# Optimization experiments

Measured on AMD Instinct MI355X. Metric: run time of the kernel, lower is better.

The kernel has to match this reference:

```python
import jax, jax.numpy as jnp
import numpy as np

T = 16384      # total packed tokens
C = 1024       # d_model
H = 16         # n_head
HD = C // H    # head dim = 64
N_SEG = 32     # number of equal varlen segments
SEG = T // N_SEG


def setup_inputs() -> dict:
    key = jax.random.key(0)
    k1, k2, k3 = jax.random.split(key, 3)
    x = jax.random.normal(k1, (T, C), dtype=jnp.float32)
    w_attn = jax.random.normal(k2, (C, 3 * C), dtype=jnp.float32) * (1.0 / np.sqrt(C))
    w_proj = jax.random.normal(k3, (C, C), dtype=jnp.float32) * (1.0 / np.sqrt(C))
    # boundary indices for torch.tensor_split -> 32 equal segments of SEG tokens
    split_sections = (jnp.arange(1, N_SEG) * SEG).astype(jnp.int64)
    return {"x": x, "w_attn": w_attn, "w_proj": w_proj, "split_sections": split_sections}


def reference(x, w_attn, w_proj, split_sections):
    # x: [T, C] packed tokens; split_sections: 31 boundaries -> 32 equal segments
    n_seg = int(np.asarray(split_sections).shape[0]) + 1
    seg = x.shape[0] // n_seg
    qkv = x @ w_attn                                   # [T, 3C]
    q, k, v = jnp.split(qkv, 3, axis=-1)               # each [T, C]

    def heads(t):
        # [T, C] -> [H, n_seg, seg, HD]  (block-diagonal segment layout)
        return t.reshape(x.shape[0], H, HD).transpose(1, 0, 2).reshape(H, n_seg, seg, HD)

    q, k, v = heads(q), heads(k), heads(v)
    scale = 1.0 / np.sqrt(HD)
    att = jnp.einsum('hnqd,hnkd->hnqk', q, k) * scale  # [H, n_seg, seg, seg]
    att = jax.nn.softmax(att, axis=-1)
    y = jnp.einsum('hnqk,hnkd->hnqd', att, v)          # [H, n_seg, seg, HD]
    y = y.reshape(H, x.shape[0], HD).transpose(1, 0, 2).reshape(x.shape[0], C)
    return y @ w_proj                                  # [T, C]
```

## Files before the change

### kernel.cpp

```cpp
#include <hip/hip_runtime.h>
#include <hip/hip_bf16.h>
#include <stdint.h>

typedef __attribute__((ext_vector_type(8))) short short8;
typedef __attribute__((ext_vector_type(4))) short short4_t;
typedef __attribute__((ext_vector_type(4))) float float4_t;

#define GLOAD_LDS16(gp, lp)                                                              \
  __builtin_amdgcn_global_load_lds((const __attribute__((address_space(1))) unsigned int*)(gp), \
                                   (__attribute__((address_space(3))) unsigned int*)(lp), \
                                   16, 0, 0)

__device__ __forceinline__ float4_t mfma_bf16(short8 a, short8 b, float4_t c) {
  return __builtin_amdgcn_mfma_f32_16x16x32_bf16(a, b, c, 0, 0, 0);
}

__device__ __forceinline__ short f2bf(float f) {
  union { float f; unsigned int u; } v; v.f = f;
  unsigned int r = v.u + 0x7fff + ((v.u >> 16) & 1);
  return (short)(r >> 16);
}

__device__ __forceinline__ float red_sum16(float v) {
  v += __shfl_xor(v, 1);
  v += __shfl_xor(v, 2);
  v += __shfl_xor(v, 4);
  v += __shfl_xor(v, 8);
  return v;
}

__device__ __forceinline__ long swz_col(long colbase64, int chunk, int sub, int row) {
  return colbase64 + ((chunk ^ (row & 7)) << 3) + sub;
}

__global__ __launch_bounds__(256) void conv_swz(const float* __restrict__ in,
                                                short* __restrict__ out, long nchunks) {
  for (long ch = (long)blockIdx.x * blockDim.x + threadIdx.x; ch < nchunks;
       ch += (long)gridDim.x * blockDim.x) {
    long r  = ch >> 7;
    int cir = (int)(ch & 127);
    int pc  = (cir & ~7) | ((cir & 7) ^ ((int)r & 7));
    const float* src = in + ch * 8;
    short8 o;
#pragma unroll
    for (int j = 0; j < 8; ++j) o[j] = f2bf(src[j]);
    *(short8*)&out[r * 1024 + pc * 8] = o;
  }
}

template <int SWZ64>
__global__ __launch_bounds__(256) void transpose_conv(const float* __restrict__ in,
                                                      short* __restrict__ out,
                                                      int R, int C) {
  __shared__ short tile[32][33];
  int c0 = blockIdx.x * 32;
  int r0 = blockIdx.y * 32;
  int tx = threadIdx.x;
  int ty = threadIdx.y;
#pragma unroll
  for (int i = 0; i < 4; ++i)
    tile[ty + i * 8][tx] = f2bf(in[(long)(r0 + ty + i * 8) * C + c0 + tx]);
  __syncthreads();
#pragma unroll
  for (int i = 0; i < 4; ++i) {
    int n   = c0 + ty + i * 8;
    int col = r0 + tx;
    long cc;
    if constexpr (SWZ64) {
      cc = swz_col((long)(col & ~63), (col >> 3) & 7, col & 7, n);
    } else {
      cc = (long)r0 + ((((tx >> 3) ^ ((n >> 1) & 3))) << 3) + (tx & 7);
    }
    out[(long)n * R + cc] = tile[tx][ty + i * 8];
  }
}

__global__ __launch_bounds__(256, 2) void gemm_bt(const short* __restrict__ A, long lda,
                                                  const short* __restrict__ Bt,
                                                  short* __restrict__ Cq,
                                                  short* __restrict__ vT,
                                                  int M, int N, int K) {
  __shared__ __align__(16) short As[128 * 64];
  __shared__ __align__(16) short Bs[128 * 64];

  const int tid  = threadIdx.x;
  const int wave = tid >> 6;
  const int lane = tid & 63;
  const int rA   = lane & 15;
  const int q4   = lane >> 4;
  const long m0  = (long)blockIdx.y * 128;
  const long n0  = (long)blockIdx.x * 128;
  const int wm   = (wave & 1) * 64;
  const int wn   = (wave >> 1) * 64;

  float4_t acc[4][4];
#pragma unroll
  for (int i = 0; i < 4; ++i)
#pragma unroll
    for (int j = 0; j < 4; ++j) acc[i][j] = (float4_t){0.f, 0.f, 0.f, 0.f};

  for (int k0 = 0; k0 < K; k0 += 64) {
#pragma unroll
    for (int i = 0; i < 4; ++i) {
      int slot = i * 256 + tid;
      int r    = slot >> 3;
      int c    = slot & 7;
      const short* ga = A  + (m0 + r) * lda      + k0 + c * 8;
      const short* gb = Bt + (n0 + r) * (long)K  + k0 + c * 8;
      GLOAD_LDS16(ga, &As[(i * 256 + wave * 64) * 8]);
      GLOAD_LDS16(gb, &Bs[(i * 256 + wave * 64) * 8]);
    }
    __syncthreads();
#pragma unroll
    for (int kk = 0; kk < 2; ++kk) {
      int cp = (kk * 4 + q4) ^ (rA & 7);
      short8 af[4], bfr[4];
#pragma unroll
      for (int mi = 0; mi < 4; ++mi) {
        int r  = wm + mi * 16 + rA;
        af[mi] = *(const short8*)&As[(r * 8 + cp) * 8];
      }
#pragma unroll
      for (int ni = 0; ni < 4; ++ni) {
        int r  = wn + ni * 16 + rA;
        bfr[ni] = *(const short8*)&Bs[(r * 8 + cp) * 8];
      }
#pragma unroll
      for (int mi = 0; mi < 4; ++mi)
#pragma unroll
        for (int ni = 0; ni < 4; ++ni)
          acc[mi][ni] = mfma_bf16(af[mi], bfr[ni], acc[mi][ni]);
    }
    __syncthreads();
  }

  if (n0 >= 2048) {
#pragma unroll
    for (int mi = 0; mi < 4; ++mi) {
      int tbase = (int)m0 + wm + mi * 16 + q4 * 4;
      int ct    = (tbase >> 3) & 7;
#pragma unroll
      for (int ni = 0; ni < 4; ++ni) {
        int c = (int)n0 + wn + ni * 16 + rA;
        int d = c - 2048;
        long dst = (long)d * 16384 + (long)(tbase & ~63) +
                   (((ct ^ (d & 7))) << 3) + (tbase & 7);
        short4_t o;
#pragma unroll
        for (int reg = 0; reg < 4; ++reg) o[reg] = f2bf(acc[mi][ni][reg]);
        *(short4_t*)&vT[dst] = o;
      }
    }
  } else {
#pragma unroll
    for (int mi = 0; mi < 4; ++mi)
#pragma unroll
      for (int ni = 0; ni < 4; ++ni)
#pragma unroll
        for (int reg = 0; reg < 4; ++reg) {
          long t = m0 + wm + mi * 16 + q4 * 4 + reg;
          int  c = (int)n0 + wn + ni * 16 + rA;
          long cc = swz_col((long)(c & ~63), (c >> 3) & 7, c & 7, (int)t);
          Cq[t * 3072 + cc] = f2bf(acc[mi][ni][reg]);
        }
  }
}

__global__ __launch_bounds__(512, 2) void gemm256(const short* __restrict__ A, long lda,
                                                  const short* __restrict__ Bt, long ldb,
                                                  float* __restrict__ Co,
                                                  int M, int N, int K) {
  __shared__ __align__(16) short As[4][256 * 32];
  __shared__ __align__(16) short Bs[4][256 * 32];

  const int tid  = threadIdx.x;
  const int wave = tid >> 6;
  const int lane = tid & 63;
  const int rA   = lane & 15;
  const int q4   = lane >> 4;
  const int wm   = (wave >> 2) * 128;
  const int wn   = (wave & 3) * 64;

  const int nbx = N >> 8;
  const int nwg = nbx * (M >> 8);
  const int bid = (int)blockIdx.y * nbx + (int)blockIdx.x;
  const int cpx = nwg >> 3;
  const int swz = (bid & 7) * cpx + (bid >> 3);
  const long m0 = (long)(swz / nbx) * 256;
  const long n0 = (long)(swz % nbx) * 256;

  const short* Ag = A  + (m0 + (tid >> 2)) * lda + (tid & 3) * 8;
  const short* Bg = Bt + (n0 + (tid >> 2)) * ldb + (tid & 3) * 8;

#define STAGE_A(u)                                                          \
  {                                                                         \
    const int slot_ = (u) & 3;                                              \
    GLOAD_LDS16(Ag + (u) * 32,             &As[slot_][wave * 512]);         \
    GLOAD_LDS16(Ag + 128 * lda + (u) * 32, &As[slot_][4096 + wave * 512]);  \
  }
#define STAGE_B(u)                                                          \
  {                                                                         \
    const int slot_ = (u) & 3;                                              \
    GLOAD_LDS16(Bg + (u) * 32,             &Bs[slot_][wave * 512]);         \
    GLOAD_LDS16(Bg + 128 * ldb + (u) * 32, &Bs[slot_][4096 + wave * 512]);  \
  }

  float4_t acc[8][4];
#pragma unroll
  for (int i = 0; i < 8; ++i)
#pragma unroll
    for (int j = 0; j < 4; ++j) acc[i][j] = (float4_t){0.f, 0.f, 0.f, 0.f};

  const int nt = K >> 5;
  const int cswz = q4 ^ ((rA >> 1) & 3);

  STAGE_A(0); STAGE_B(0);
  STAGE_A(1); STAGE_B(1);
  STAGE_A(2); STAGE_B(2);
  asm volatile("s_waitcnt vmcnt(8)" ::: "memory");
  __builtin_amdgcn_s_barrier();

  short8 afl[4], afh[4], bf0[4], bf1[4];
#pragma unroll
  for (int mi = 0; mi < 4; ++mi)
    afl[mi] = *(const short8*)&As[0][((wm + mi * 16 + rA) * 4 + cswz) * 8];
#pragma unroll
  for (int ni = 0; ni < 4; ++ni)
    bf0[ni] = *(const short8*)&Bs[0][((wn + ni * 16 + rA) * 4 + cswz) * 8];

  auto tile_step = [&](int u, short8 (&bc)[4], short8 (&bn)[4]) {
    const int slot = u & 3;
#pragma unroll
    for (int mi = 0; mi < 4; ++mi)
      afh[mi] = *(const short8*)&As[slot][((wm + 64 + mi * 16 + rA) * 4 + cswz) * 8];
    if (u + 3 < nt) STAGE_A(u + 3);
    asm volatile("s_waitcnt lgkmcnt(4)" ::: "memory");
    __builtin_amdgcn_s_setprio(1);
#pragma unroll
    for (int mi = 0; mi < 4; ++mi)
#pragma unroll
      for (int ni = 0; ni < 4; ++ni)
        acc[mi][ni] = mfma_bf16(afl[mi], bc[ni], acc[mi][ni]);
    __builtin_amdgcn_s_setprio(0);
    if (u + 3 < nt)      asm volatile("s_waitcnt vmcnt(6)" ::: "memory");
    else if (u + 2 < nt) asm volatile("s_waitcnt vmcnt(4)" ::: "memory");
    else                 asm volatile("s_waitcnt vmcnt(0)" ::: "memory");
    __builtin_amdgcn_s_barrier();
    if (u + 1 < nt) {
      const int ns = (u + 1) & 3;
#pragma unroll
      for (int mi = 0; mi < 4; ++mi)
        afl[mi] = *(const short8*)&As[ns][((wm + mi * 16 + rA) * 4 + cswz) * 8];
#pragma unroll
      for (int ni = 0; ni < 4; ++ni)
        bn[ni] = *(const short8*)&Bs[ns][((wn + ni * 16 + rA) * 4 + cswz) * 8];
    }
    if (u + 3 < nt) STAGE_B(u + 3);
    if (u + 1 < nt) asm volatile("s_waitcnt lgkmcnt(8)" ::: "memory");
    else            asm volatile("s_waitcnt lgkmcnt(0)" ::: "memory");
    __builtin_amdgcn_s_setprio(1);
#pragma unroll
    for (int mi = 0; mi < 4; ++mi)
#pragma unroll
      for (int ni = 0; ni < 4; ++ni)
        acc[mi + 4][ni] = mfma_bf16(afh[mi], bc[ni], acc[mi + 4][ni]);
    __builtin_amdgcn_s_setprio(0);
    __builtin_amdgcn_s_barrier();
  };

  for (int u = 0; u < nt; u += 2) {
    tile_step(u,     bf0, bf1);
    tile_step(u + 1, bf1, bf0);
  }
#undef STAGE_A
#undef STAGE_B

#pragma unroll
  for (int mi = 0; mi < 8; ++mi)
#pragma unroll
    for (int ni = 0; ni < 4; ++ni)
#pragma unroll
      for (int reg = 0; reg < 4; ++reg) {
        long row = m0 + wm + mi * 16 + q4 * 4 + reg;
        long col = n0 + wn + ni * 16 + rA;
        Co[row * (long)N + col] = acc[mi][ni][reg];
      }
}

__global__ __launch_bounds__(256, 2) void attn_kernel(short* __restrict__ qkv,
                                                      const short* __restrict__ vT) {
  __shared__ __align__(16) short Qs[128 * 64];
  __shared__ __align__(16) short Ks[2][64 * 64];
  __shared__ __align__(16) short Vt[2][64 * 64];
  __shared__ __align__(16) short Ps[128 * 72];

  const int tid  = threadIdx.x;
  const int wave = tid >> 6;
  const int lane = tid & 63;
  const int rA   = lane & 15;
  const int q4   = lane >> 4;
  const int qt   = blockIdx.x;
  const int seg  = blockIdx.y;
  const int h    = blockIdx.z;

  const long tq0  = (long)seg * 512 + qt * 128;
  const long tk0  = (long)seg * 512;
  const long hoff = (long)h * 64;

#pragma unroll
  for (int i = 0; i < 4; ++i) {
    int slot = i * 256 + tid;
    int r    = slot >> 3;
    int c    = slot & 7;
    GLOAD_LDS16(qkv + (tq0 + r) * 3072 + hoff + c * 8, &Qs[(i * 256 + wave * 64) * 8]);
  }
#pragma unroll
  for (int i = 0; i < 2; ++i) {
    int slot = i * 256 + tid;
    int r    = slot >> 3;
    int c    = slot & 7;
    GLOAD_LDS16(qkv + (tk0 + r) * 3072 + 1024 + hoff + c * 8,
                &Ks[0][(i * 256 + wave * 64) * 8]);
    GLOAD_LDS16(vT + (hoff + r) * 16384 + tk0 + c * 8,
                &Vt[0][(i * 256 + wave * 64) * 8]);
  }

  float4_t acc_o[2][4];
  float l_st[2][4];
#pragma unroll
  for (int mi = 0; mi < 2; ++mi)
#pragma unroll
    for (int di = 0; di < 4; ++di) acc_o[mi][di] = (float4_t){0.f, 0.f, 0.f, 0.f};
#pragma unroll
  for (int mi = 0; mi < 2; ++mi)
#pragma unroll
    for (int reg = 0; reg < 4; ++reg) l_st[mi][reg] = 0.f;

  for (int kt = 0; kt < 8; ++kt) {
    const int p = kt & 1;
    __syncthreads();

    if (kt < 7) {
      const long tkn = tk0 + (kt + 1) * 64;
#pragma unroll
      for (int i = 0; i < 2; ++i) {
        int slot = i * 256 + tid;
        int r    = slot >> 3;
        int c    = slot & 7;
        GLOAD_LDS16(qkv + (tkn + r) * 3072 + 1024 + hoff + c * 8,
                    &Ks[1 - p][(i * 256 + wave * 64) * 8]);
        GLOAD_LDS16(vT + (hoff + r) * 16384 + tkn + c * 8,
                    &Vt[1 - p][(i * 256 + wave * 64) * 8]);
      }
    }

    float4_t s_acc[2][4];
#pragma unroll
    for (int mi = 0; mi < 2; ++mi)
#pragma unroll
      for (int ni = 0; ni < 4; ++ni) s_acc[mi][ni] = (float4_t){0.f, 0.f, 0.f, 0.f};
#pragma unroll
    for (int kk = 0; kk < 2; ++kk) {
      int cp = (kk * 4 + q4) ^ (rA & 7);
      short8 af[2], bfr[4];
#pragma unroll
      for (int mi = 0; mi < 2; ++mi) {
        int r  = wave * 32 + mi * 16 + rA;
        af[mi] = *(const short8*)&Qs[(r * 8 + cp) * 8];
      }
#pragma unroll
      for (int ni = 0; ni < 4; ++ni) {
        int r  = ni * 16 + rA;
        bfr[ni] = *(const short8*)&Ks[p][(r * 8 + cp) * 8];
      }
#pragma unroll
      for (int mi = 0; mi < 2; ++mi)
#pragma unroll
        for (int ni = 0; ni < 4; ++ni)
          s_acc[mi][ni] = mfma_bf16(af[mi], bfr[ni], s_acc[mi][ni]);
    }

#pragma unroll
    for (int mi = 0; mi < 2; ++mi)
#pragma unroll
      for (int reg = 0; reg < 4; ++reg) {
        float rs = 0.f;
#pragma unroll
        for (int ni = 0; ni < 4; ++ni) {
          float pv = __expf(s_acc[mi][ni][reg] * 0.125f);
          s_acc[mi][ni][reg] = pv;
          rs += pv;
        }
        l_st[mi][reg] += rs;
      }

#pragma unroll
    for (int mi = 0; mi < 2; ++mi)
#pragma unroll
      for (int ni = 0; ni < 4; ++ni)
#pragma unroll
        for (int reg = 0; reg < 4; ++reg)
          Ps[(wave * 32 + mi * 16 + q4 * 4 + reg) * 72 + ni * 16 + rA] =
              f2bf(s_acc[mi][ni][reg]);

    __syncthreads();

#pragma unroll
    for (int kk = 0; kk < 2; ++kk) {
      int cp = (kk * 4 + q4) ^ (rA & 7);
      short8 af[2], bfr[4];
#pragma unroll
      for (int mi = 0; mi < 2; ++mi)
        af[mi] = *(const short8*)&Ps[(wave * 32 + mi * 16 + rA) * 72 + (kk * 4 + q4) * 8];
#pragma unroll
      for (int di = 0; di < 4; ++di)
        bfr[di] = *(const short8*)&Vt[p][((di * 16 + rA) * 8 + cp) * 8];
#pragma unroll
      for (int mi = 0; mi < 2; ++mi)
#pragma unroll
        for (int di = 0; di < 4; ++di)
          acc_o[mi][di] = mfma_bf16(af[mi], bfr[di], acc_o[mi][di]);
    }
  }

#pragma unroll
  for (int mi = 0; mi < 2; ++mi)
#pragma unroll
    for (int reg = 0; reg < 4; ++reg) {
      float l  = red_sum16(l_st[mi][reg]);
      float rl = 1.0f / l;
      long t = tq0 + wave * 32 + mi * 16 + q4 * 4 + reg;
#pragma unroll
      for (int di = 0; di < 4; ++di) {
        int c  = di * 16 + rA;
        long cc = hoff + (c & 32) +
                  (((((c >> 3) & 3) ^ (((int)t >> 1) & 3))) << 3) + (c & 7);
        qkv[t * 3072 + cc] = f2bf(acc_o[mi][di][reg] * rl);
      }
    }
}

extern "C" void kernel_launch(void* const* d_in, const int* in_sizes, int n_in,
                              void* d_out, int out_size, void* d_ws, size_t ws_size,
                              hipStream_t stream) {
  const float* x      = (const float*)d_in[0];
  const float* w_attn = (const float*)d_in[1];
  const float* w_proj = (const float*)d_in[2];
  float* out = (float*)d_out;

  short* wT_a = (short*)d_ws;
  short* wT_p = wT_a + (size_t)3072 * 1024;
  short* qkv  = wT_p + (size_t)1024 * 1024;

  short* xb = (short*)d_out;
  short* vT = xb + (size_t)16384 * 1024;

  conv_swz<<<2048, 256, 0, stream>>>(x, xb, (long)16384 * 1024 / 8);
  transpose_conv<1><<<dim3(3072 / 32, 1024 / 32), dim3(32, 8), 0, stream>>>(w_attn, wT_a, 1024, 3072);
  transpose_conv<0><<<dim3(1024 / 32, 1024 / 32), dim3(32, 8), 0, stream>>>(w_proj, wT_p, 1024, 1024);

  gemm_bt<<<dim3(3072 / 128, 16384 / 128), 256, 0, stream>>>(xb, 1024, wT_a, qkv, vT,
                                                             16384, 3072, 1024);

  attn_kernel<<<dim3(4, 32, 16), 256, 0, stream>>>(qkv, vT);

  gemm256<<<dim3(1024 / 256, 16384 / 256), 512, 0, stream>>>(qkv, 3072, wT_p, 1024, out,
                                                             16384, 1024, 1024);
}
```

Baseline: 357.3 us.

## Process whole segment per attention block with 512 threads and swizzled P tile

The attention kernel now launches one 512-thread block per (segment, head) instead of four 128-query blocks, so each K/V tile loaded into LDS is reused by all 512 query rows. Each wave handles 64 query rows, the P buffer uses an XOR-swizzled layout instead of padding, and MFMA sections are wrapped in s_setprio. The V tile is now single-buffered and fetched at the start of each iteration rather than prefetched a step ahead, and the much larger LDS footprint with a quarter as many blocks reduces occupancy and can expose load latency.

Result: no change. 359.8 us (+0.7%).

```diff
diff --git a/kernel.cpp b/kernel.cpp
--- a/kernel.cpp
+++ b/kernel.cpp
@@ -287,52 +287,46 @@
       }
 }
 
-__global__ __launch_bounds__(256, 2) void attn_kernel(short* __restrict__ qkv,
+__global__ __launch_bounds__(512, 2) void attn_kernel(short* __restrict__ qkv,
                                                       const short* __restrict__ vT) {
-  __shared__ __align__(16) short Qs[128 * 64];
+  __shared__ __align__(16) short Qs[512 * 64];
   __shared__ __align__(16) short Ks[2][64 * 64];
-  __shared__ __align__(16) short Vt[2][64 * 64];
-  __shared__ __align__(16) short Ps[128 * 72];
+  __shared__ __align__(16) short Vt[64 * 64];
+  __shared__ __align__(16) short Ps[512 * 64];
 
   const int tid  = threadIdx.x;
   const int wave = tid >> 6;
   const int lane = tid & 63;
   const int rA   = lane & 15;
   const int q4   = lane >> 4;
-  const int qt   = blockIdx.x;
-  const int seg  = blockIdx.y;
-  const int h    = blockIdx.z;
-
-  const long tq0  = (long)seg * 512 + qt * 128;
+  const int seg  = blockIdx.x;
+  const int h    = blockIdx.y;
+
+  const long tq0  = (long)seg * 512;
   const long tk0  = (long)seg * 512;
   const long hoff = (long)h * 64;
 
 #pragma unroll
-  for (int i = 0; i < 4; ++i) {
-    int slot = i * 256 + tid;
+  for (int i = 0; i < 8; ++i) {
+    int slot = i * 512 + tid;
     int r    = slot >> 3;
     int c    = slot & 7;
-    GLOAD_LDS16(qkv + (tq0 + r) * 3072 + hoff + c * 8, &Qs[(i * 256 + wave * 64) * 8]);
-  }
-#pragma unroll
-  for (int i = 0; i < 2; ++i) {
-    int slot = i * 256 + tid;
-    int r    = slot >> 3;
-    int c    = slot & 7;
-    GLOAD_LDS16(qkv + (tk0 + r) * 3072 + 1024 + hoff + c * 8,
-                &Ks[0][(i * 256 + wave * 64) * 8]);
-    GLOAD_LDS16(vT + (hoff + r) * 16384 + tk0 + c * 8,
-                &Vt[0][(i * 256 + wave * 64) * 8]);
-  }
-
-  float4_t acc_o[2][4];
-  float l_st[2][4];
-#pragma unroll
-  for (int mi = 0; mi < 2; ++mi)
+    GLOAD_LDS16(qkv + (tq0 + r) * 3072 + hoff + c * 8, &Qs[(i * 512 + wave * 64) * 8]);
+  }
+  {
+    int r = tid >> 3;
+    int c = tid & 7;
+    GLOAD_LDS16(qkv + (tk0 + r) * 3072 + 1024 + hoff + c * 8, &Ks[0][(wave * 64) * 8]);
+  }
+
+  float4_t acc_o[4][4];
+  float l_st[4][4];
+#pragma unroll
+  for (int mi = 0; mi < 4; ++mi)
 #pragma unroll
     for (int di = 0; di < 4; ++di) acc_o[mi][di] = (float4_t){0.f, 0.f, 0.f, 0.f};
 #pragma unroll
-  for (int mi = 0; mi < 2; ++mi)
+  for (int mi = 0; mi < 4; ++mi)
 #pragma unroll
     for (int reg = 0; reg < 4; ++reg) l_st[mi][reg] = 0.f;
 
@@ -340,32 +334,27 @@
     const int p = kt & 1;
     __syncthreads();
 
-    if (kt < 7) {
-      const long tkn = tk0 + (kt + 1) * 64;
-#pragma unroll
-      for (int i = 0; i < 2; ++i) {
-        int slot = i * 256 + tid;
-        int r    = slot >> 3;
-        int c    = slot & 7;
-        GLOAD_LDS16(qkv + (tkn + r) * 3072 + 1024 + hoff + c * 8,
-                    &Ks[1 - p][(i * 256 + wave * 64) * 8]);
-        GLOAD_LDS16(vT + (hoff + r) * 16384 + tkn + c * 8,
-                    &Vt[1 - p][(i * 256 + wave * 64) * 8]);
-      }
-    }
-
-    float4_t s_acc[2][4];
-#pragma unroll
-    for (int mi = 0; mi < 2; ++mi)
+    {
+      int r = tid >> 3;
+      int c = tid & 7;
+      GLOAD_LDS16(vT + (hoff + r) * 16384 + tk0 + kt * 64 + c * 8, &Vt[(wave * 64) * 8]);
+      if (kt < 7)
+        GLOAD_LDS16(qkv + (tk0 + (kt + 1) * 64 + r) * 3072 + 1024 + hoff + c * 8,
+                    &Ks[1 - p][(wave * 64) * 8]);
+    }
+
+    float4_t s_acc[4][4];
+#pragma unroll
+    for (int mi = 0; mi < 4; ++mi)
 #pragma unroll
       for (int ni = 0; ni < 4; ++ni) s_acc[mi][ni] = (float4_t){0.f, 0.f, 0.f, 0.f};
 #pragma unroll
     for (int kk = 0; kk < 2; ++kk) {
       int cp = (kk * 4 + q4) ^ (rA & 7);
-      short8 af[2], bfr[4];
-#pragma unroll
-      for (int mi = 0; mi < 2; ++mi) {
-        int r  = wave * 32 + mi * 16 + rA;
+      short8 af[4], bfr[4];
+#pragma unroll
+      for (int mi = 0; mi < 4; ++mi) {
+        int r  = wave * 64 + mi * 16 + rA;
         af[mi] = *(const short8*)&Qs[(r * 8 + cp) * 8];
       }
 #pragma unroll
@@ -373,15 +362,17 @@
         int r  = ni * 16 + rA;
         bfr[ni] = *(const short8*)&Ks[p][(r * 8 + cp) * 8];
       }
-#pragma unroll
-      for (int mi = 0; mi < 2; ++mi)
+      __builtin_amdgcn_s_setprio(1);
+#pragma unroll
+      for (int mi = 0; mi < 4; ++mi)
 #pragma unroll
         for (int ni = 0; ni < 4; ++ni)
           s_acc[mi][ni] = mfma_bf16(af[mi], bfr[ni], s_acc[mi][ni]);
-    }
-
-#pragma unroll
-    for (int mi = 0; mi < 2; ++mi)
+      __builtin_amdgcn_s_setprio(0);
+    }
+
+#pragma unroll
+    for (int mi = 0; mi < 4; ++mi)
 #pragma unroll
       for (int reg = 0; reg < 4; ++reg) {
         float rs = 0.f;
@@ -395,41 +386,48 @@
       }
 
 #pragma unroll
-    for (int mi = 0; mi < 2; ++mi)
+    for (int mi = 0; mi < 4; ++mi)
 #pragma unroll
       for (int ni = 0; ni < 4; ++ni)
 #pragma unroll
-        for (int reg = 0; reg < 4; ++reg)
-          Ps[(wave * 32 + mi * 16 + q4 * 4 + reg) * 72 + ni * 16 + rA] =
+        for (int reg = 0; reg < 4; ++reg) {
+          int row = wave * 64 + mi * 16 + q4 * 4 + reg;
+          int col = ni * 16 + rA;
+          Ps[row * 64 + (((col >> 3) ^ (row & 7)) << 3) + (col & 7)] =
               f2bf(s_acc[mi][ni][reg]);
+        }
 
     __syncthreads();
 
 #pragma unroll
     for (int kk = 0; kk < 2; ++kk) {
       int cp = (kk * 4 + q4) ^ (rA & 7);
-      short8 af[2], bfr[4];
-#pragma unroll
-      for (int mi = 0; mi < 2; ++mi)
-        af[mi] = *(const short8*)&Ps[(wave * 32 + mi * 16 + rA) * 72 + (kk * 4 + q4) * 8];
+      short8 af[4], bfr[4];
+#pragma unroll
+      for (int mi = 0; mi < 4; ++mi) {
+        int row = wave * 64 + mi * 16 + rA;
+        af[mi] = *(const short8*)&Ps[row * 64 + cp * 8];
+      }
 #pragma unroll
       for (int di = 0; di < 4; ++di)
-        bfr[di] = *(const short8*)&Vt[p][((di * 16 + rA) * 8 + cp) * 8];
-#pragma unroll
-      for (int mi = 0; mi < 2; ++mi)
+        bfr[di] = *(const short8*)&Vt[((di * 16 + rA) * 8 + cp) * 8];
+      __builtin_amdgcn_s_setprio(1);
+#pragma unroll
+      for (int mi = 0; mi < 4; ++mi)
 #pragma unroll
         for (int di = 0; di < 4; ++di)
           acc_o[mi][di] = mfma_bf16(af[mi], bfr[di], acc_o[mi][di]);
-    }
-  }
-
-#pragma unroll
-  for (int mi = 0; mi < 2; ++mi)
+      __builtin_amdgcn_s_setprio(0);
+    }
+  }
+
+#pragma unroll
+  for (int mi = 0; mi < 4; ++mi)
 #pragma unroll
     for (int reg = 0; reg < 4; ++reg) {
       float l  = red_sum16(l_st[mi][reg]);
       float rl = 1.0f / l;
-      long t = tq0 + wave * 32 + mi * 16 + q4 * 4 + reg;
+      long t = tq0 + wave * 64 + mi * 16 + q4 * 4 + reg;
 #pragma unroll
       for (int di = 0; di < 4; ++di) {
         int c  = di * 16 + rA;
@@ -462,7 +460,7 @@
   gemm_bt<<<dim3(3072 / 128, 16384 / 128), 256, 0, stream>>>(xb, 1024, wT_a, qkv, vT,
                                                              16384, 3072, 1024);
 
-  attn_kernel<<<dim3(4, 32, 16), 256, 0, stream>>>(qkv, vT);
+  attn_kernel<<<dim3(32, 16), 512, 0, stream>>>(qkv, vT);
 
   gemm256<<<dim3(1024 / 256, 16384 / 256), 512, 0, stream>>>(qkv, 3072, wT_p, 1024, out,
                                                              16384, 1024, 1024);
```
